# Kernel tuning notes

Hardware: AMD Instinct MI355X
Metric: run time of the kernel (lower is better)

## Reference

```python
import jax, jax.numpy as jnp
import numpy as np
from jax import lax

T, B, E, U, V = 512, 256, 512, 1024, 50257
H1, H2, L = 512, 256, 2


def setup_inputs() -> dict:
    key = jax.random.key(0)
    ks = jax.random.split(key, 12)
    s = lambda n: 1.0 / np.sqrt(n)
    return {
        "inputs": jax.random.randint(ks[0], (T, B), 0, V, dtype=jnp.int32),
        "input_lengths": jax.random.randint(ks[1], (B,), 1, T + 1, dtype=jnp.int32),
        "embedder": jax.random.normal(ks[2], (V, E), jnp.float32),
        # GRU params (TF GRUCell layout: gates over [x, h] -> 2U; candidate over [x, r*h] -> U)
        "W_gates": jax.random.normal(ks[3], (E + U, 2 * U), jnp.float32) * s(E + U),
        "b_gates": jnp.ones((2 * U,), jnp.float32),  # TF bias init 1.0
        "W_cand": jax.random.normal(ks[4], (E + U, U), jnp.float32) * s(E + U),
        "b_cand": jnp.zeros((U,), jnp.float32),
        # MLP (fully_connected default activation = relu; final layer linear)
        "W1": jax.random.normal(ks[5], (U, H1), jnp.float32) * s(U),
        "b1": jnp.zeros((H1,), jnp.float32),
        "W2": jax.random.normal(ks[6], (H1, H2), jnp.float32) * s(H1),
        "b2": jnp.zeros((H2,), jnp.float32),
        "W3": jax.random.normal(ks[7], (H2, L), jnp.float32) * s(H2),
        "b3": jnp.zeros((L,), jnp.float32),
    }


def reference(inputs, input_lengths, embedder, W_gates, b_gates, W_cand, b_cand,
              W1, b1, W2, b2, W3, b3):
    emb = embedder[inputs]  # [T, B, E] (time-major, as in batch_embedding_lookup)
    t_idx = jnp.arange(emb.shape[0], dtype=input_lengths.dtype)

    def step(h, xt):
        x, t = xt
        xh = jnp.concatenate([x, h], axis=-1)                      # [B, E+U]
        r, z = jnp.split(jax.nn.sigmoid(xh @ W_gates + b_gates), 2, axis=-1)
        cand = jnp.tanh(jnp.concatenate([x, r * h], axis=-1) @ W_cand + b_cand)
        h_new = z * h + (1.0 - z) * cand                           # TF GRUCell update
        # dynamic_rnn sequence_length semantics: state held past end of sequence
        h_out = jnp.where((t < input_lengths)[:, None], h_new, h)
        return h_out, None

    h0 = jnp.zeros((emb.shape[1], U), emb.dtype)
    h_final, _ = lax.scan(step, h0, (emb, t_idx))                  # [B, U]

    x = jax.nn.relu(h_final @ W1 + b1)
    x = jax.nn.relu(x @ W2 + b2)
    logits = x @ W3 + b3                                           # [B, 2]
    predictions = jax.nn.softmax(logits, axis=-1)
    return logits, predictions
```

## Files before the change

kernel.cpp:

```cpp
#include <hip/hip_runtime.h>

typedef unsigned short u16;
typedef unsigned int u32;
typedef unsigned long long u64;

using bf16x8 = __attribute__((ext_vector_type(8))) __bf16;
using f32x4  = __attribute__((ext_vector_type(4))) float;

#define T_DIM 512
#define B_DIM 256
#define E_DIM 512
#define U_DIM 1024
#define K_DIM 1536
#define NG    2048
#define NWG   256

__device__ __forceinline__ u16 f2bf(float f) {
  union { float f; u32 u; } v; v.f = f;
  return (u16)((v.u + 0x7fffu + ((v.u >> 16) & 1u)) >> 16);
}

#define WAIT_VM_ALL() do { asm volatile("s_waitcnt vmcnt(0)" ::: "memory"); \
                           __builtin_amdgcn_sched_barrier(0); } while (0)

#define LD16T(dst, base, OFS) \
  asm volatile("global_load_dwordx4 %0, %1, off offset:" #OFS " sc0 sc1" \
               : "=&v"(dst) : "v"(base))

#define LOAD32T(arr, b) do { \
  const u16* _b0 = (b);           const u16* _b1 = (b) + 2048;  \
  const u16* _b2 = (b) + 4096;    const u16* _b3 = (b) + 6144;  \
  const u16* _b4 = (b) + 8192;    const u16* _b5 = (b) + 10240; \
  const u16* _b6 = (b) + 12288;   const u16* _b7 = (b) + 14336; \
  LD16T(arr[0],  _b0, 0); LD16T(arr[1],  _b0, 1024); \
  LD16T(arr[2],  _b0, 2048); LD16T(arr[3],  _b0, 3072); \
  LD16T(arr[4],  _b1, 0); LD16T(arr[5],  _b1, 1024); \
  LD16T(arr[6],  _b1, 2048); LD16T(arr[7],  _b1, 3072); \
  LD16T(arr[8],  _b2, 0); LD16T(arr[9],  _b2, 1024); \
  LD16T(arr[10], _b2, 2048); LD16T(arr[11], _b2, 3072); \
  LD16T(arr[12], _b3, 0); LD16T(arr[13], _b3, 1024); \
  LD16T(arr[14], _b3, 2048); LD16T(arr[15], _b3, 3072); \
  LD16T(arr[16], _b4, 0); LD16T(arr[17], _b4, 1024); \
  LD16T(arr[18], _b4, 2048); LD16T(arr[19], _b4, 3072); \
  LD16T(arr[20], _b5, 0); LD16T(arr[21], _b5, 1024); \
  LD16T(arr[22], _b5, 2048); LD16T(arr[23], _b5, 3072); \
  LD16T(arr[24], _b6, 0); LD16T(arr[25], _b6, 1024); \
  LD16T(arr[26], _b6, 2048); LD16T(arr[27], _b6, 3072); \
  LD16T(arr[28], _b7, 0); LD16T(arr[29], _b7, 1024); \
  LD16T(arr[30], _b7, 2048); LD16T(arr[31], _b7, 3072); \
} while (0)

__device__ __forceinline__ void st_u64_coh(u64* p, u64 v) {
  u64 r = __hip_atomic_exchange(p, v, __ATOMIC_RELAXED,
                                __HIP_MEMORY_SCOPE_AGENT);
  asm volatile("" :: "v"(r));
}

__global__ __launch_bounds__(256) void init_kernel(float* hF, u16* hB, int* bar) {
  int i = blockIdx.x * 256 + threadIdx.x;
  hF[i] = 0.f;
  hB[i] = 0;
  if (i < 8192) bar[i] = 0;
}

__global__ __launch_bounds__(256) void wconv_kernel(const float* __restrict__ W,
                                                    u16* __restrict__ Wt, int N) {
  int k = blockIdx.x * 64 + (threadIdx.x & 63);
  int n = blockIdx.y * 4 + (threadIdx.x >> 6);
  Wt[(size_t)n * K_DIM + k] = f2bf(W[(size_t)k * N + n]);
}

__global__ __launch_bounds__(128) void embed_kernel(const int* __restrict__ inp,
                                                    const float* __restrict__ emb,
                                                    u16* __restrict__ X) {
  int rb = blockIdx.x;
  int idx = inp[rb];
  int e = threadIdx.x * 4;
  float4 v = *(const float4*)&emb[(size_t)idx * E_DIM + e];
  ushort4 o;
  o.x = f2bf(v.x); o.y = f2bf(v.y); o.z = f2bf(v.z); o.w = f2bf(v.w);
  *(ushort4*)&X[(size_t)rb * E_DIM + e] = o;
}

__device__ __forceinline__ bf16x8 ldsW(const u16* Wl, int lc, int k) {
  int ofs = lc * 3072 + k * 2;
  ofs ^= ((lc & 7) << 4);
  return *(const bf16x8*)((const char*)Wl + ofs);
}

__device__ __forceinline__ void barrier_arrive(int* fbase, int ct, int phase) {
  if (threadIdx.x == 0) {
    int r = __hip_atomic_exchange(&fbase[ct * 32], phase, __ATOMIC_RELAXED,
                                  __HIP_MEMORY_SCOPE_AGENT);
    asm volatile("" :: "v"(r));
  }
}
__device__ __forceinline__ int barrier_wait(int* fbase, int phase,
                                            int* sh_tok) {
  if (threadIdx.x < 64) {
    int v;
    do {
      v = __hip_atomic_load(&fbase[threadIdx.x * 32], __ATOMIC_RELAXED,
                            __HIP_MEMORY_SCOPE_AGENT);
      if (v >= phase) break;
      __builtin_amdgcn_s_sleep(1);
    } while (true);
    if (threadIdx.x == 0) *sh_tok = (v >> 30);
  }
  __syncthreads();
  return *sh_tok;
}

__global__ void __launch_bounds__(256, 1) gru_loop(
    const u16* __restrict__ X, const u16* __restrict__ WgT,
    const u16* __restrict__ WcT, const float* __restrict__ bg,
    const float* __restrict__ bc, float* __restrict__ hF,
    u16* __restrict__ hB, u16* __restrict__ rhB,
    const int* __restrict__ lens, int* bar) {
  __shared__ __align__(16) u16 Wl[48 * K_DIM];
  __shared__ int sh_tok;
  const int tid = threadIdx.x;
  const int wgid = blockIdx.x;
  const int ct = wgid >> 2;
  const int mq = wgid & 3;

#pragma unroll 4
  for (int it = 0; it < 36; ++it) {
    int ci = it * 256 + tid;
    int lc = ci / 192;
    int k0 = (ci - lc * 192) * 8;
    const u16* src = (lc < 16)
        ? WgT + (size_t)(ct * 16 + lc) * K_DIM + k0
        : (lc < 32)
          ? WgT + (size_t)(1024 + ct * 16 + (lc - 16)) * K_DIM + k0
          : WcT + (size_t)(ct * 16 + (lc - 32)) * K_DIM + k0;
    uint4 v = *(const uint4*)src;
    int ofs = lc * 3072 + k0 * 2;
    ofs ^= ((lc & 7) << 4);
    *(uint4*)((char*)Wl + ofs) = v;
  }
  __syncthreads();

  const int lane = tid & 63, wv = tid >> 6;
  const int l15 = lane & 15;
  const int kq8 = (lane >> 4) * 8;
  const int lq4 = (lane >> 4) * 4;
  const int rbase = mq * 64 + wv * 16;
  const int tbase = (rbase >> 4) * 16384 + (lane >> 4) * 128 + l15 * 8;
  const u16* Hp = hB + tbase;
  const u16* Rp = rhB + tbase;
  int* fbase = bar + mq * 2048;

  int len4[4];
#pragma unroll
  for (int q = 0; q < 4; ++q) len4[q] = lens[rbase + lq4 + q];
  const int nc = ct * 16 + l15;
  const float bg0 = bg[nc];
  const float bg1 = bg[1024 + nc];
  const float bc0 = bc[nc];
  u16* rhW = rhB + (rbase >> 4) * 16384 + (nc >> 3) * 128 + (nc & 7);
  u16* hW  = hB  + (rbase >> 4) * 16384 + (nc >> 3) * 128 + (nc & 7);

  float h_reg[4] = {0.f, 0.f, 0.f, 0.f};
  float z_reg[4];

  bf16x8 af[16], ah[32];
  int phase = 0;
  int tok = 0;
  for (int t = 0; t < T_DIM; ++t) {
    const u16* HpT = Hp + tok;
    LOAD32T(ah, HpT);
    const u16* Xt = X + ((size_t)t * B_DIM + rbase + l15) * E_DIM + kq8;
#pragma unroll
    for (int kb = 0; kb < 16; ++kb) af[kb] = *(const bf16x8*)(Xt + kb * 32);
    WAIT_VM_ALL();

    f32x4 a0 = {0.f, 0.f, 0.f, 0.f}, a1 = {0.f, 0.f, 0.f, 0.f};
#pragma unroll
    for (int kb = 0; kb < 48; ++kb) {
      bf16x8 av = (kb < 16) ? af[kb] : ah[kb - 16];
      bf16x8 b0 = ldsW(Wl, l15, kb * 32 + kq8);
      bf16x8 b1 = ldsW(Wl, 16 + l15, kb * 32 + kq8);
      a0 = __builtin_amdgcn_mfma_f32_16x16x32_bf16(av, b0, a0, 0, 0, 0);
      a1 = __builtin_amdgcn_mfma_f32_16x16x32_bf16(av, b1, a1, 0, 0, 0);
    }
#pragma unroll
    for (int q = 0; q < 4; ++q) {
      float r = 1.f / (1.f + __expf(-(a0[q] + bg0)));
      z_reg[q] = 1.f / (1.f + __expf(-(a1[q] + bg1)));
      u16 rv = f2bf(r * h_reg[q]);
      u32 lo = (u32)rv | ((u32)(u16)__shfl_xor((int)rv, 1) << 16);
      u32 hi = (u32)__shfl_xor((int)lo, 2);
      if ((l15 & 3) == 0) {
        st_u64_coh((u64*)(rhW + (lq4 + q) * 8), (u64)lo | ((u64)hi << 32));
      }
    }
    __syncthreads();
    barrier_arrive(fbase, ct, ++phase);
    f32x4 a2 = {0.f, 0.f, 0.f, 0.f};
#pragma unroll
    for (int kb = 0; kb < 16; ++kb) {
      bf16x8 b2 = ldsW(Wl, 32 + l15, kb * 32 + kq8);
      a2 = __builtin_amdgcn_mfma_f32_16x16x32_bf16(af[kb], b2, a2, 0, 0, 0);
    }
    tok = barrier_wait(fbase, phase, &sh_tok);

    const u16* RpT = Rp + tok;
    LOAD32T(ah, RpT);
    WAIT_VM_ALL();
#pragma unroll
    for (int kb = 0; kb < 32; ++kb) {
      bf16x8 b2 = ldsW(Wl, 32 + l15, (kb + 16) * 32 + kq8);
      a2 = __builtin_amdgcn_mfma_f32_16x16x32_bf16(ah[kb], b2, a2, 0, 0, 0);
    }
#pragma unroll
    for (int q = 0; q < 4; ++q) {
      int row = rbase + lq4 + q;
      float c = tanhf(a2[q] + bc0);
      float hn = z_reg[q] * h_reg[q] + (1.f - z_reg[q]) * c;
      float v = (t < len4[q]) ? hn : h_reg[q];
      h_reg[q] = v;
      u16 hv = f2bf(v);
      u32 lo = (u32)hv | ((u32)(u16)__shfl_xor((int)hv, 1) << 16);
      u32 hi = (u32)__shfl_xor((int)lo, 2);
      if ((l15 & 3) == 0) {
        st_u64_coh((u64*)(hW + (lq4 + q) * 8), (u64)lo | ((u64)hi << 32));
      }
      if (t == T_DIM - 1) {
        hF[(size_t)row * U_DIM + nc] = v;
      }
    }
    __syncthreads();
    barrier_arrive(fbase, ct, ++phase);
    tok = barrier_wait(fbase, phase, &sh_tok);
  }
}

__global__ __launch_bounds__(256) void mlp1_kernel(const float* __restrict__ h,
                                                   const float* __restrict__ W1,
                                                   const float* __restrict__ b1,
                                                   float* __restrict__ o1) {
  int m = blockIdx.x, tid = threadIdx.x;
  __shared__ float xs[1024];
  for (int k = tid; k < 1024; k += 256) xs[k] = h[(size_t)m * 1024 + k];
  __syncthreads();
  for (int n = tid; n < 512; n += 256) {
    float s = b1[n];
    for (int k = 0; k < 1024; ++k) s += xs[k] * W1[(size_t)k * 512 + n];
    o1[(size_t)m * 512 + n] = fmaxf(s, 0.f);
  }
}

__global__ __launch_bounds__(256) void mlp2_kernel(const float* __restrict__ x,
                                                   const float* __restrict__ W2,
                                                   const float* __restrict__ b2,
                                                   float* __restrict__ o2) {
  int m = blockIdx.x, tid = threadIdx.x;
  __shared__ float xs[512];
  for (int k = tid; k < 512; k += 256) xs[k] = x[(size_t)m * 512 + k];
  __syncthreads();
  int n = tid;
  float s = b2[n];
  for (int k = 0; k < 512; ++k) s += xs[k] * W2[(size_t)k * 256 + n];
  o2[(size_t)m * 256 + n] = fmaxf(s, 0.f);
}

__global__ __launch_bounds__(256) void mlp3_kernel(const float* __restrict__ x,
                                                   const float* __restrict__ W3,
                                                   const float* __restrict__ b3,
                                                   float* __restrict__ out) {
  int m = blockIdx.x, tid = threadIdx.x;
  float xk = x[(size_t)m * 256 + tid];
  float p0 = xk * W3[tid * 2 + 0];
  float p1 = xk * W3[tid * 2 + 1];
#pragma unroll
  for (int off = 32; off; off >>= 1) {
    p0 += __shfl_down(p0, off);
    p1 += __shfl_down(p1, off);
  }
  __shared__ float s0[4], s1[4];
  int wave = tid >> 6, lane = tid & 63;
  if (lane == 0) { s0[wave] = p0; s1[wave] = p1; }
  __syncthreads();
  if (tid == 0) {
    float l0 = s0[0] + s0[1] + s0[2] + s0[3] + b3[0];
    float l1 = s1[0] + s1[1] + s1[2] + s1[3] + b3[1];
    out[m * 2 + 0] = l0;
    out[m * 2 + 1] = l1;
    float mx = fmaxf(l0, l1);
    float e0 = __expf(l0 - mx), e1 = __expf(l1 - mx);
    float inv = 1.f / (e0 + e1);
    out[512 + m * 2 + 0] = e0 * inv;
    out[512 + m * 2 + 1] = e1 * inv;
  }
}

extern "C" void kernel_launch(void* const* d_in, const int* in_sizes, int n_in,
                              void* d_out, int out_size, void* d_ws, size_t ws_size,
                              hipStream_t stream) {
  (void)in_sizes; (void)n_in; (void)out_size; (void)ws_size;
  const int* inputs = (const int*)d_in[0];
  const int* lens = (const int*)d_in[1];
  const float* embedder = (const float*)d_in[2];
  const float* Wg = (const float*)d_in[3];
  const float* bg = (const float*)d_in[4];
  const float* Wc = (const float*)d_in[5];
  const float* bc = (const float*)d_in[6];
  const float* W1 = (const float*)d_in[7];
  const float* b1 = (const float*)d_in[8];
  const float* W2 = (const float*)d_in[9];
  const float* b2 = (const float*)d_in[10];
  const float* W3 = (const float*)d_in[11];
  const float* b3 = (const float*)d_in[12];
  float* out = (float*)d_out;

  char* ws = (char*)d_ws;
  size_t off = 0;
  u16* X = (u16*)(ws + off);       off += (size_t)T_DIM * B_DIM * E_DIM * 2;
  u16* WgT = (u16*)(ws + off);     off += (size_t)NG * K_DIM * 2;
  u16* WcT = (u16*)(ws + off);     off += (size_t)U_DIM * K_DIM * 2;
  float* hF = (float*)(ws + off);  off += (size_t)B_DIM * U_DIM * 4;
  u16* hB = (u16*)(ws + off);      off += (size_t)B_DIM * U_DIM * 2;
  u16* rhB = (u16*)(ws + off);     off += (size_t)B_DIM * U_DIM * 2;
  float* o1 = (float*)(ws + off);  off += (size_t)B_DIM * 512 * 4;
  float* o2 = (float*)(ws + off);  off += (size_t)B_DIM * 256 * 4;
  int* bar = (int*)(ws + off);     off += 65536;

  init_kernel<<<dim3(1024), dim3(256), 0, stream>>>(hF, hB, bar);
  wconv_kernel<<<dim3(24, 512), dim3(256), 0, stream>>>(Wg, WgT, NG);
  wconv_kernel<<<dim3(24, 256), dim3(256), 0, stream>>>(Wc, WcT, U_DIM);
  embed_kernel<<<dim3(T_DIM * B_DIM), dim3(128), 0, stream>>>(inputs, embedder, X);

  gru_loop<<<dim3(NWG), dim3(256), 0, stream>>>(X, WgT, WcT, bg, bc, hF, hB, rhB,
                                                lens, bar);

  mlp1_kernel<<<dim3(256), dim3(256), 0, stream>>>(hF, W1, b1, o1);
  mlp2_kernel<<<dim3(256), dim3(256), 0, stream>>>(o1, W2, b2, o2);
  mlp3_kernel<<<dim3(256), dim3(256), 0, stream>>>(o2, W3, b3, out);
}
```

Before: 7.104 ms.

## Shorten GRU critical path with per-wave arrivals and reordered gate GEMMs

Replaces the workgroup-wide __syncthreads plus single-thread flag with per-wave arrival flags, so each wave signals as soon as its own stores finish. The barrier wait now polls 256 flags, one per thread. Only the r-gate GEMM stays on the critical path before the rh publication; the z-gate GEMM is moved after the arrive. The x-part of the next step's r-gate GEMM, including the X load, is computed while waiting on the second barrier. This trades more flag traffic and polling for a shorter dependency chain per step.

```diff
diff --git a/kernel.cpp b/kernel.cpp
--- a/kernel.cpp
+++ b/kernel.cpp
@@ -88,25 +88,25 @@
   return *(const bf16x8*)((const char*)Wl + ofs);
 }
 
-__device__ __forceinline__ void barrier_arrive(int* fbase, int ct, int phase) {
-  if (threadIdx.x == 0) {
-    int r = __hip_atomic_exchange(&fbase[ct * 32], phase, __ATOMIC_RELAXED,
-                                  __HIP_MEMORY_SCOPE_AGENT);
+__device__ __forceinline__ void wave_arrive(int* fbase, int ct, int wv,
+                                            int phase, int lane) {
+  WAIT_VM_ALL();
+  if (lane == 0) {
+    int r = __hip_atomic_exchange(&fbase[(ct * 4 + wv) * 8], phase,
+                                  __ATOMIC_RELAXED, __HIP_MEMORY_SCOPE_AGENT);
     asm volatile("" :: "v"(r));
   }
 }
 __device__ __forceinline__ int barrier_wait(int* fbase, int phase,
                                             int* sh_tok) {
-  if (threadIdx.x < 64) {
-    int v;
-    do {
-      v = __hip_atomic_load(&fbase[threadIdx.x * 32], __ATOMIC_RELAXED,
-                            __HIP_MEMORY_SCOPE_AGENT);
-      if (v >= phase) break;
-      __builtin_amdgcn_s_sleep(1);
-    } while (true);
-    if (threadIdx.x == 0) *sh_tok = (v >> 30);
-  }
+  int v;
+  do {
+    v = __hip_atomic_load(&fbase[threadIdx.x * 8], __ATOMIC_RELAXED,
+                          __HIP_MEMORY_SCOPE_AGENT);
+    if (v >= phase) break;
+    __builtin_amdgcn_s_sleep(1);
+  } while (true);
+  if (threadIdx.x == 0) *sh_tok = (v >> 30);
   __syncthreads();
   return *sh_tok;
 }
@@ -165,29 +165,33 @@
   float z_reg[4];
 
   bf16x8 af[16], ah[32];
+  f32x4 a0 = {0.f, 0.f, 0.f, 0.f};
+  {
+    const u16* Xt = X + ((size_t)0 * B_DIM + rbase + l15) * E_DIM + kq8;
+#pragma unroll
+    for (int kb = 0; kb < 16; ++kb) af[kb] = *(const bf16x8*)(Xt + kb * 32);
+    WAIT_VM_ALL();
+#pragma unroll
+    for (int kb = 0; kb < 16; ++kb) {
+      a0 = __builtin_amdgcn_mfma_f32_16x16x32_bf16(af[kb],
+              ldsW(Wl, l15, kb * 32 + kq8), a0, 0, 0, 0);
+    }
+  }
+
   int phase = 0;
   int tok = 0;
   for (int t = 0; t < T_DIM; ++t) {
     const u16* HpT = Hp + tok;
     LOAD32T(ah, HpT);
-    const u16* Xt = X + ((size_t)t * B_DIM + rbase + l15) * E_DIM + kq8;
-#pragma unroll
-    for (int kb = 0; kb < 16; ++kb) af[kb] = *(const bf16x8*)(Xt + kb * 32);
     WAIT_VM_ALL();
-
-    f32x4 a0 = {0.f, 0.f, 0.f, 0.f}, a1 = {0.f, 0.f, 0.f, 0.f};
-#pragma unroll
-    for (int kb = 0; kb < 48; ++kb) {
-      bf16x8 av = (kb < 16) ? af[kb] : ah[kb - 16];
-      bf16x8 b0 = ldsW(Wl, l15, kb * 32 + kq8);
-      bf16x8 b1 = ldsW(Wl, 16 + l15, kb * 32 + kq8);
-      a0 = __builtin_amdgcn_mfma_f32_16x16x32_bf16(av, b0, a0, 0, 0, 0);
-      a1 = __builtin_amdgcn_mfma_f32_16x16x32_bf16(av, b1, a1, 0, 0, 0);
+#pragma unroll
+    for (int kb = 0; kb < 32; ++kb) {
+      a0 = __builtin_amdgcn_mfma_f32_16x16x32_bf16(ah[kb],
+              ldsW(Wl, l15, (kb + 16) * 32 + kq8), a0, 0, 0, 0);
     }
 #pragma unroll
     for (int q = 0; q < 4; ++q) {
       float r = 1.f / (1.f + __expf(-(a0[q] + bg0)));
-      z_reg[q] = 1.f / (1.f + __expf(-(a1[q] + bg1)));
       u16 rv = f2bf(r * h_reg[q]);
       u32 lo = (u32)rv | ((u32)(u16)__shfl_xor((int)rv, 1) << 16);
       u32 hi = (u32)__shfl_xor((int)lo, 2);
@@ -195,13 +199,26 @@
         st_u64_coh((u64*)(rhW + (lq4 + q) * 8), (u64)lo | ((u64)hi << 32));
       }
     }
-    __syncthreads();
-    barrier_arrive(fbase, ct, ++phase);
+    wave_arrive(fbase, ct, wv, ++phase, lane);
+    f32x4 a1 = {0.f, 0.f, 0.f, 0.f};
+#pragma unroll
+    for (int kb = 0; kb < 16; ++kb) {
+      a1 = __builtin_amdgcn_mfma_f32_16x16x32_bf16(af[kb],
+              ldsW(Wl, 16 + l15, kb * 32 + kq8), a1, 0, 0, 0);
+    }
+#pragma unroll
+    for (int kb = 0; kb < 32; ++kb) {
+      a1 = __builtin_amdgcn_mfma_f32_16x16x32_bf16(ah[kb],
+              ldsW(Wl, 16 + l15, (kb + 16) * 32 + kq8), a1, 0, 0, 0);
+    }
+#pragma unroll
+    for (int q = 0; q < 4; ++q)
+      z_reg[q] = 1.f / (1.f + __expf(-(a1[q] + bg1)));
     f32x4 a2 = {0.f, 0.f, 0.f, 0.f};
 #pragma unroll
     for (int kb = 0; kb < 16; ++kb) {
-      bf16x8 b2 = ldsW(Wl, 32 + l15, kb * 32 + kq8);
-      a2 = __builtin_amdgcn_mfma_f32_16x16x32_bf16(af[kb], b2, a2, 0, 0, 0);
+      a2 = __builtin_amdgcn_mfma_f32_16x16x32_bf16(af[kb],
+              ldsW(Wl, 32 + l15, kb * 32 + kq8), a2, 0, 0, 0);
     }
     tok = barrier_wait(fbase, phase, &sh_tok);
 
@@ -210,8 +227,8 @@
     WAIT_VM_ALL();
 #pragma unroll
     for (int kb = 0; kb < 32; ++kb) {
-      bf16x8 b2 = ldsW(Wl, 32 + l15, (kb + 16) * 32 + kq8);
-      a2 = __builtin_amdgcn_mfma_f32_16x16x32_bf16(ah[kb], b2, a2, 0, 0, 0);
+      a2 = __builtin_amdgcn_mfma_f32_16x16x32_bf16(ah[kb],
+              ldsW(Wl, 32 + l15, (kb + 16) * 32 + kq8), a2, 0, 0, 0);
     }
 #pragma unroll
     for (int q = 0; q < 4; ++q) {
@@ -230,8 +247,19 @@
         hF[(size_t)row * U_DIM + nc] = v;
       }
     }
-    __syncthreads();
-    barrier_arrive(fbase, ct, ++phase);
+    wave_arrive(fbase, ct, wv, ++phase, lane);
+    a0 = f32x4{0.f, 0.f, 0.f, 0.f};
+    if (t + 1 < T_DIM) {
+      const u16* Xt = X + ((size_t)(t + 1) * B_DIM + rbase + l15) * E_DIM + kq8;
+#pragma unroll
+      for (int kb = 0; kb < 16; ++kb) af[kb] = *(const bf16x8*)(Xt + kb * 32);
+      WAIT_VM_ALL();
+#pragma unroll
+      for (int kb = 0; kb < 16; ++kb) {
+        a0 = __builtin_amdgcn_mfma_f32_16x16x32_bf16(af[kb],
+                ldsW(Wl, l15, kb * 32 + kq8), a0, 0, 0, 0);
+      }
+    }
     tok = barrier_wait(fbase, phase, &sh_tok);
   }
 }
```

New measurement: 7.050 ms, median of 2. Within noise of the previous version (-0.8%).
